# Kernel optimization log

Hardware: AMD Instinct MI355X
Metric: run time of the kernel (lower is better)

Reference implementation:

```python
import jax, jax.numpy as jnp
import numpy as np

D_IN = 1024
D_OUT = 1024
N_HEADS = 16
HEAD_DIM = D_IN // N_HEADS


def setup_inputs() -> dict:
    key = jax.random.key(0)
    k0, k1, k2, k3, k4, k5 = jax.random.split(key, 6)
    s = 1.0 / np.sqrt(D_IN)
    return {
        "input_embeddings": jax.random.normal(k0, (4, 2048, D_IN), dtype=jnp.float32),
        "Wq": jax.random.normal(k1, (D_IN, D_IN), dtype=jnp.float32) * s,
        "Wk": jax.random.normal(k2, (D_IN, D_IN), dtype=jnp.float32) * s,
        "Wv": jax.random.normal(k3, (D_IN, D_IN), dtype=jnp.float32) * s,
        "Wo": jax.random.normal(k4, (D_IN, D_OUT), dtype=jnp.float32) * s,
        "bo": jax.random.normal(k5, (D_OUT,), dtype=jnp.float32) * 0.01,
    }


def reference(input_embeddings, Wq, Wk, Wv, Wo, bo):
    B, T, D = input_embeddings.shape
    x = input_embeddings
    # QKV projections (no bias), split into heads: (B, H, T, hd)
    def split(y):
        return y.reshape(B, T, N_HEADS, HEAD_DIM).transpose(0, 2, 1, 3)
    Q = split(x @ Wq)
    K = split(x @ Wk)
    V = split(x @ Wv)
    scale = 1.0 / np.sqrt(HEAD_DIM)
    scores = jnp.einsum("bhqd,bhkd->bhqk", Q, K) * scale  # (B,H,T,T)
    causal = jnp.tril(jnp.ones((T, T), dtype=bool))
    scores = jnp.where(causal, scores, -jnp.inf)
    probs = jax.nn.softmax(scores, axis=-1)  # dropout p=0 -> identity
    out = jnp.einsum("bhqk,bhkd->bhqd", probs, V)
    out = out.transpose(0, 2, 1, 3).reshape(B, T, D)
    return out @ Wo + bo
```

## Files before the change

### kernel.cpp

```cpp
#include <hip/hip_runtime.h>
#include <hip/hip_bf16.h>
#include <math.h>

typedef __attribute__((ext_vector_type(8))) short short8;
typedef __attribute__((ext_vector_type(4))) float f32x4;

#define MFMA_BF16 __builtin_amdgcn_mfma_f32_16x16x32_bf16

static constexpr int Dm = 1024;
static constexpr int Tm = 2048;
static constexpr int Bb = 4;
static constexpr int NHm = 16;
static constexpr int HDm = 64;
static constexpr int Mtot = Bb * Tm;
static constexpr int NKT = Tm / 64;
static constexpr float kQScale = 0.125f * 1.4426950408889634f;

__device__ __forceinline__ unsigned short f2bf(float f) {
  unsigned int u = __float_as_uint(f);
  u += 0x7FFFu + ((u >> 16) & 1u);
  return (unsigned short)(u >> 16);
}

__device__ __forceinline__ float fexp2(float x) {
  float r;
  asm("v_exp_f32 %0, %1" : "=v"(r) : "v"(x));
  return r;
}

__device__ __forceinline__ void gload16(const void* g, void* l) {
  __builtin_amdgcn_global_load_lds((const __attribute__((address_space(1))) void*)g,
                                   (__attribute__((address_space(3))) void*)l, 16, 0, 0);
}

__global__ __launch_bounds__(256) void cvt_kernel(const float* __restrict__ src,
                                                  short* __restrict__ dst, int n) {
  int stride = gridDim.x * blockDim.x;
  for (int i = blockIdx.x * blockDim.x + threadIdx.x; i * 4 < n; i += stride) {
    float4 v = reinterpret_cast<const float4*>(src)[i];
    short4 o;
    o.x = (short)f2bf(v.x);
    o.y = (short)f2bf(v.y);
    o.z = (short)f2bf(v.z);
    o.w = (short)f2bf(v.w);
    reinterpret_cast<short4*>(dst)[i] = o;
  }
}

__global__ __launch_bounds__(256) void cvt_t_kernel(
    const float* __restrict__ W0, const float* __restrict__ W1,
    const float* __restrict__ W2, const float* __restrict__ W3,
    short* __restrict__ T0, short* __restrict__ T1,
    short* __restrict__ T2, short* __restrict__ T3) {
  const float* W = blockIdx.z == 0 ? W0 : blockIdx.z == 1 ? W1 : blockIdx.z == 2 ? W2 : W3;
  short* Wt = blockIdx.z == 0 ? T0 : blockIdx.z == 1 ? T1 : blockIdx.z == 2 ? T2 : T3;
  __shared__ __align__(16) short T[64 * 72];
  const int tid = threadIdx.x;
  const int k0 = blockIdx.y * 64, n0 = blockIdx.x * 64;
#pragma unroll
  for (int p = 0; p < 4; ++p) {
    int idx = tid + p * 256;
    int kr = idx >> 4, c4 = (idx & 15) * 4;
    float4 v = *reinterpret_cast<const float4*>(W + (size_t)(k0 + kr) * Dm + n0 + c4);
    T[(c4 + 0) * 72 + kr] = (short)f2bf(v.x);
    T[(c4 + 1) * 72 + kr] = (short)f2bf(v.y);
    T[(c4 + 2) * 72 + kr] = (short)f2bf(v.z);
    T[(c4 + 3) * 72 + kr] = (short)f2bf(v.w);
  }
  __syncthreads();
#pragma unroll
  for (int p = 0; p < 2; ++p) {
    int idx = tid + p * 256;
    int nr = idx >> 3, c8 = (idx & 7) * 8;
    *reinterpret_cast<short8*>(Wt + (size_t)(n0 + nr) * Dm + k0 + c8) =
        *reinterpret_cast<const short8*>(&T[nr * 72 + c8]);
  }
}

__device__ __forceinline__ void gemm_mainloop2(
    const short* __restrict__ A, const short* __restrict__ B,
    int m0, int n0, short* As, short* Bs, f32x4 acc[4][4], int tid) {
  const int lane = tid & 63;
  const int w = tid >> 6;
  const int wr = (w >> 1) * 64, wc = (w & 1) * 64;
  const int lr = lane & 15;
  const int g = lane >> 4;
  const int rowt = tid >> 2;
  const int csw = ((tid & 3) ^ ((tid >> 3) & 3)) * 8;

  auto stage = [&](int kt, int buf) {
#pragma unroll
    for (int p = 0; p < 2; ++p) {
      gload16(A + (size_t)(m0 + p * 64 + rowt) * Dm + kt * 32 + csw,
              &As[buf * 4096 + (p * 64 + w * 16) * 32]);
      gload16(B + (size_t)(n0 + p * 64 + rowt) * Dm + kt * 32 + csw,
              &Bs[buf * 4096 + (p * 64 + w * 16) * 32]);
    }
  };

  const int rsw = (lr >> 1) & 3;
  const int csel = (g ^ rsw) * 8;

  stage(0, 0);
  __syncthreads();
  for (int kt = 0; kt < Dm / 32; ++kt) {
    if (kt + 1 < Dm / 32) stage(kt + 1, (kt + 1) & 1);
    __builtin_amdgcn_sched_barrier(0);
    const int cur = kt & 1;
    short8 a[4], b[4];
#pragma unroll
    for (int mi = 0; mi < 4; ++mi)
      a[mi] = *reinterpret_cast<const short8*>(
          &As[cur * 4096 + (wr + mi * 16 + lr) * 32 + csel]);
#pragma unroll
    for (int ni = 0; ni < 4; ++ni)
      b[ni] = *reinterpret_cast<const short8*>(
          &Bs[cur * 4096 + (wc + ni * 16 + lr) * 32 + csel]);
#pragma unroll
    for (int mi = 0; mi < 4; ++mi)
#pragma unroll
      for (int ni = 0; ni < 4; ++ni)
        acc[mi][ni] = MFMA_BF16(a[mi], b[ni], acc[mi][ni], 0, 0, 0);
    __syncthreads();
  }
}

__global__ __launch_bounds__(256) void gemm_qkv_kernel(
    const short* __restrict__ Ags, const short* __restrict__ WT3,
    short* __restrict__ Qo, short* __restrict__ Ko, short* __restrict__ Vo) {
  __shared__ __align__(16) short As[2 * 128 * 32];
  __shared__ __align__(16) short Bs[2 * 128 * 32];
  const int tid = threadIdx.x;
  const int m0 = blockIdx.x * 128;
  const int n0g = blockIdx.y * 128;
  const int z = n0g >> 10;
  const int n0 = n0g & 1023;
  short* Co = z == 0 ? Qo : z == 1 ? Ko : Vo;

  f32x4 acc[4][4];
#pragma unroll
  for (int mi = 0; mi < 4; ++mi)
#pragma unroll
    for (int ni = 0; ni < 4; ++ni)
#pragma unroll
      for (int r = 0; r < 4; ++r) acc[mi][ni][r] = 0.f;

  gemm_mainloop2(Ags, WT3, m0, n0g, As, Bs, acc, tid);

  const int lane = tid & 63;
  const int w = tid >> 6;
  const int wr = (w >> 1) * 64, wc = (w & 1) * 64;
  const int g = lane >> 4, lr = lane & 15;
#pragma unroll
  for (int mi = 0; mi < 4; ++mi)
#pragma unroll
    for (int ni = 0; ni < 4; ++ni)
#pragma unroll
      for (int r = 0; r < 4; ++r) {
        int mg = m0 + wr + mi * 16 + g * 4 + r;
        int ng = n0 + wc + ni * 16 + lr;
        float v = acc[mi][ni][r];
        int b_ = mg >> 11, t_ = mg & 2047, h_ = ng >> 6, d_ = ng & 63;
        size_t bh = (size_t)(b_ * NHm + h_);
        if (z == 0) {
          Co[(bh * Tm + t_) * HDm + d_] = (short)f2bf(v * kQScale);
        } else if (z == 1) {
          Co[((bh * NKT + (t_ >> 6)) << 12) + (t_ & 63) * 64 + (d_ ^ ((t_ & 7) << 3))] =
              (short)f2bf(v);
        } else {
          Co[((bh * NKT + (t_ >> 6)) << 12) + d_ * 64 + ((t_ & 63) ^ ((d_ & 7) << 3))] =
              (short)f2bf(v);
        }
      }
}

__global__ __launch_bounds__(256) void gemm_out_kernel(
    const short* __restrict__ Ags, const short* __restrict__ Bts,
    float* __restrict__ Cf, const float* __restrict__ bias) {
  __shared__ __align__(16) short As[2 * 128 * 32];
  __shared__ __align__(16) short Bs[2 * 128 * 32];
  const int tid = threadIdx.x;
  const int m0 = blockIdx.x * 128;
  const int n0 = blockIdx.y * 128;

  f32x4 acc[4][4];
#pragma unroll
  for (int mi = 0; mi < 4; ++mi)
#pragma unroll
    for (int ni = 0; ni < 4; ++ni)
#pragma unroll
      for (int r = 0; r < 4; ++r) acc[mi][ni][r] = 0.f;

  gemm_mainloop2(Ags, Bts, m0, n0, As, Bs, acc, tid);

  const int lane = tid & 63;
  const int w = tid >> 6;
  const int wr = (w >> 1) * 64, wc = (w & 1) * 64;
  const int g = lane >> 4, lr = lane & 15;
#pragma unroll
  for (int mi = 0; mi < 4; ++mi)
#pragma unroll
    for (int ni = 0; ni < 4; ++ni)
#pragma unroll
      for (int r = 0; r < 4; ++r) {
        int mg = m0 + wr + mi * 16 + g * 4 + r;
        int ng = n0 + wc + ni * 16 + lr;
        Cf[(size_t)mg * Dm + ng] = acc[mi][ni][r] + bias[ng];
      }
}

__global__ __launch_bounds__(256) void attn_kernel(
    const short* __restrict__ Qg, const short* __restrict__ Kg,
    const short* __restrict__ Vg, short* __restrict__ Og) {
  __shared__ __align__(16) short Kl[3][64 * 64];
  __shared__ __align__(16) short Vl[3][64 * 64];
  __shared__ __align__(16) short Pl[4][32 * 72];
  const int tid = threadIdx.x;
  const int lane = tid & 63;
  const int w = tid >> 6;
  const int g = lane >> 4;
  const int lr = lane & 15;
  const int bh = blockIdx.x;
  const int pi = blockIdx.y;
  const short* Ks = Kg + ((size_t)bh * NKT << 12);
  const short* Vs = Vg + ((size_t)bh * NKT << 12);
  short* Pw = &Pl[w][0];
  const int b_ = bh >> 4, h_ = bh & 15;

  short8 ones;
#pragma unroll
  for (int j = 0; j < 8; ++j) ones[j] = (short)0x3F80;

  auto stage = [&](int t, int buf) {
#pragma unroll
    for (int i = 0; i < 2; ++i) {
      int ch = w * 2 + i;
      gload16(Ks + ((size_t)t << 12) + ch * 512 + lane * 8, &Kl[buf][ch * 512]);
      gload16(Vs + ((size_t)t << 12) + ch * 512 + lane * 8, &Vl[buf][ch * 512]);
    }
  };

  for (int pass = 0; pass < 2; ++pass) {
    const int qb = pass == 0 ? (15 - pi) : pi;
    const int q0 = qb * 128;
    const int qw = q0 + w * 32;
    const short* Qs = Qg + ((size_t)bh * Tm + q0) * HDm;

    short8 qf[2][2];
#pragma unroll
    for (int mi = 0; mi < 2; ++mi)
#pragma unroll
      for (int kk = 0; kk < 2; ++kk)
        qf[mi][kk] = *reinterpret_cast<const short8*>(
            Qs + (w * 32 + mi * 16 + lr) * HDm + kk * 32 + g * 8);

    f32x4 o[2][4], lacc[2];
#pragma unroll
    for (int mi = 0; mi < 2; ++mi)
#pragma unroll
      for (int r = 0; r < 4; ++r) {
        lacc[mi][r] = 0.f;
#pragma unroll
        for (int di = 0; di < 4; ++di) o[mi][di][r] = 0.f;
      }

    const int nt = q0 / 64 + 2;
    stage(0, 0);
    stage(1, 1);
    for (int t = 0; t < nt; ++t) {
      if (t < nt - 1) asm volatile("s_waitcnt vmcnt(4)" ::: "memory");
      else            asm volatile("s_waitcnt vmcnt(0)" ::: "memory");
      __builtin_amdgcn_s_barrier();
      __builtin_amdgcn_sched_barrier(0);
      if (t + 2 < nt) stage(t + 2, (t + 2) % 3);
      const int cur = t % 3;
      const int k0 = t * 64;
      const bool active = (k0 <= qw + 31);
      if (active) {
        short8 kf[2][4];
#pragma unroll
        for (int ni = 0; ni < 4; ++ni) {
          int row = ni * 16 + lr;
#pragma unroll
          for (int kk = 0; kk < 2; ++kk)
            kf[kk][ni] = *reinterpret_cast<const short8*>(
                &Kl[cur][row * 64 + ((kk * 32 + g * 8) ^ ((row & 7) << 3))]);
        }
        f32x4 s[2][4];
#pragma unroll
        for (int mi = 0; mi < 2; ++mi)
#pragma unroll
          for (int ni = 0; ni < 4; ++ni) {
            f32x4 acc;
#pragma unroll
            for (int r = 0; r < 4; ++r) acc[r] = 0.f;
            acc = MFMA_BF16(qf[mi][0], kf[0][ni], acc, 0, 0, 0);
            acc = MFMA_BF16(qf[mi][1], kf[1][ni], acc, 0, 0, 0);
            s[mi][ni] = acc;
          }
        if (k0 + 63 > qw) {
#pragma unroll
          for (int mi = 0; mi < 2; ++mi)
#pragma unroll
            for (int ni = 0; ni < 4; ++ni)
#pragma unroll
              for (int r = 0; r < 4; ++r)
                if (k0 + ni * 16 + lr > qw + mi * 16 + g * 4 + r) s[mi][ni][r] = -1e30f;
        }
#pragma unroll
        for (int mi = 0; mi < 2; ++mi)
#pragma unroll
          for (int ni = 0; ni < 4; ++ni)
#pragma unroll
            for (int r = 0; r < 4; ++r)
              Pw[(mi * 16 + g * 4 + r) * 72 + ((ni * 16 + lr) ^ (g << 4))] =
                  (short)f2bf(fexp2(s[mi][ni][r]));

#pragma unroll
        for (int kk = 0; kk < 2; ++kk) {
          short8 pf[2];
#pragma unroll
          for (int mi = 0; mi < 2; ++mi)
            pf[mi] = *reinterpret_cast<const short8*>(
                &Pw[(mi * 16 + lr) * 72 + ((kk * 32 + g * 8) ^ ((lr >> 2) << 4))]);
#pragma unroll
          for (int mi = 0; mi < 2; ++mi)
            lacc[mi] = MFMA_BF16(pf[mi], ones, lacc[mi], 0, 0, 0);
#pragma unroll
          for (int di = 0; di < 4; ++di) {
            int d = di * 16 + lr;
            short8 vf = *reinterpret_cast<const short8*>(
                &Vl[cur][d * 64 + ((kk * 32 + g * 8) ^ ((d & 7) << 3))]);
#pragma unroll
            for (int mi = 0; mi < 2; ++mi)
              o[mi][di] = MFMA_BF16(pf[mi], vf, o[mi][di], 0, 0, 0);
          }
        }
      }
    }
    __syncthreads();

#pragma unroll
    for (int mi = 0; mi < 2; ++mi)
#pragma unroll
      for (int di = 0; di < 4; ++di)
#pragma unroll
        for (int r = 0; r < 4; ++r) {
          float ov = o[mi][di][r] / lacc[mi][r];
          int qg = q0 + w * 32 + mi * 16 + g * 4 + r;
          int d_ = di * 16 + lr;
          Og[((size_t)b_ * Tm + qg) * Dm + h_ * HDm + d_] = (short)f2bf(ov);
        }
  }
}

extern "C" void kernel_launch(void* const* d_in, const int* in_sizes, int n_in,
                              void* d_out, int out_size, void* d_ws, size_t ws_size,
                              hipStream_t stream) {
  const float* X = (const float*)d_in[0];
  const float* Wq = (const float*)d_in[1];
  const float* Wk = (const float*)d_in[2];
  const float* Wv = (const float*)d_in[3];
  const float* Wo = (const float*)d_in[4];
  const float* bo = (const float*)d_in[5];
  float* out = (float*)d_out;

  char* ws = (char*)d_ws;
  short* Xb = (short*)ws;  ws += (size_t)Mtot * Dm * 2;
  short* Wqt = (short*)ws; ws += (size_t)Dm * Dm * 2;
  short* Wkt = (short*)ws; ws += (size_t)Dm * Dm * 2;
  short* Wvt = (short*)ws; ws += (size_t)Dm * Dm * 2;
  short* Wot = (short*)ws; ws += (size_t)Dm * Dm * 2;
  short* Qb = (short*)ws;  ws += (size_t)Mtot * Dm * 2;
  short* Kb = (short*)ws;  ws += (size_t)Mtot * Dm * 2;
  short* Vb = (short*)ws;  ws += (size_t)Mtot * Dm * 2;
  short* Ab = (short*)ws;  ws += (size_t)Mtot * Dm * 2;

  cvt_kernel<<<dim3(1024), dim3(256), 0, stream>>>(X, Xb, Mtot * Dm);
  cvt_t_kernel<<<dim3(16, 16, 4), dim3(256), 0, stream>>>(Wq, Wk, Wv, Wo, Wqt, Wkt, Wvt, Wot);

  gemm_qkv_kernel<<<dim3(Mtot / 128, 3 * Dm / 128), 256, 0, stream>>>(
      Xb, Wqt, Qb, Kb, Vb);

  attn_kernel<<<dim3(Bb * NHm, 8), 256, 0, stream>>>(Qb, Kb, Vb, Ab);

  gemm_out_kernel<<<dim3(Mtot / 128, Dm / 128), 256, 0, stream>>>(Ab, Wot, out, bo);
}
```

Before: 192.8 us.

## Load GEMM A operands directly into registers, stage only B through LDS

The QKV and output GEMM mainloops no longer stage A tiles in shared memory. Each wave loads its A fragments straight from global memory into double-buffered registers one k-step ahead, and only B goes through LDS via async loads. Synchronisation uses explicit barriers and vmcnt waits, and launch bounds request 4 blocks per CU. This halves LDS footprint and traffic to allow higher occupancy, but A global loads are no longer shared across the two waves that use the same rows, which doubles A reads from L2.

```diff
diff --git a/kernel.cpp b/kernel.cpp
--- a/kernel.cpp
+++ b/kernel.cpp
@@ -77,9 +77,35 @@
   }
 }
 
-__device__ __forceinline__ void gemm_mainloop2(
+#define GSTEP(KT, CUR, PF)                                                    \
+  {                                                                           \
+    __builtin_amdgcn_s_barrier();  \
+    if (PF) {                                                                 \
+      _Pragma("unroll") for (int mi = 0; mi < 4; ++mi)                        \
+          a[(CUR) ^ 1][mi] = *reinterpret_cast<const short8*>(                \
+              Ar[mi] + ((KT) + 1) * 32);                                      \
+      stageB((KT) + 1, (CUR) ^ 1);                                            \
+      __builtin_amdgcn_sched_barrier(0);                                      \
+      asm volatile("s_waitcnt vmcnt(6)" ::: "memory");                        \
+    } else {                                                                  \
+      asm volatile("s_waitcnt vmcnt(0)" ::: "memory");                        \
+    }                                                                         \
+    __builtin_amdgcn_s_barrier();                        \
+    __builtin_amdgcn_sched_barrier(0);                                        \
+    short8 b[4];                                                              \
+    _Pragma("unroll") for (int ni = 0; ni < 4; ++ni)                          \
+        b[ni] = *reinterpret_cast<const short8*>(                             \
+            &Bs[(CUR) * 4096 + (wc + ni * 16 + lr) * 32 + csel]);             \
+    _Pragma("unroll") for (int mi = 0; mi < 4; ++mi)                          \
+        _Pragma("unroll") for (int ni = 0; ni < 4; ++ni)                      \
+            acc[mi][ni] =                                                     \
+                MFMA_BF16(a[CUR][mi], b[ni], acc[mi][ni], 0, 0, 0);           \
+  }
+
+__device__ __forceinline__ void gemm_mainloopA(
     const short* __restrict__ A, const short* __restrict__ B,
-    int m0, int n0, short* As, short* Bs, f32x4 acc[4][4], int tid) {
+    int m0, int n0, short* Bs, f32x4 acc[4][4], int tid) {
+  constexpr int NT = Dm / 32;
   const int lane = tid & 63;
   const int w = tid >> 6;
   const int wr = (w >> 1) * 64, wc = (w & 1) * 64;
@@ -87,48 +113,38 @@
   const int g = lane >> 4;
   const int rowt = tid >> 2;
   const int csw = ((tid & 3) ^ ((tid >> 3) & 3)) * 8;
-
-  auto stage = [&](int kt, int buf) {
-#pragma unroll
-    for (int p = 0; p < 2; ++p) {
-      gload16(A + (size_t)(m0 + p * 64 + rowt) * Dm + kt * 32 + csw,
-              &As[buf * 4096 + (p * 64 + w * 16) * 32]);
-      gload16(B + (size_t)(n0 + p * 64 + rowt) * Dm + kt * 32 + csw,
-              &Bs[buf * 4096 + (p * 64 + w * 16) * 32]);
-    }
+  const short* Bsrc0 = B + (size_t)(n0 + rowt) * Dm + csw;
+  const short* Bsrc1 = B + (size_t)(n0 + 64 + rowt) * Dm + csw;
+  short* Bd0 = Bs + (w * 16) * 32;
+  short* Bd1 = Bs + (64 + w * 16) * 32;
+  auto stageB = [&](int kt, int buf) {
+    gload16(Bsrc0 + kt * 32, Bd0 + buf * 4096);
+    gload16(Bsrc1 + kt * 32, Bd1 + buf * 4096);
   };
-
-  const int rsw = (lr >> 1) & 3;
-  const int csel = (g ^ rsw) * 8;
-
-  stage(0, 0);
-  __syncthreads();
-  for (int kt = 0; kt < Dm / 32; ++kt) {
-    if (kt + 1 < Dm / 32) stage(kt + 1, (kt + 1) & 1);
-    __builtin_amdgcn_sched_barrier(0);
-    const int cur = kt & 1;
-    short8 a[4], b[4];
-#pragma unroll
-    for (int mi = 0; mi < 4; ++mi)
-      a[mi] = *reinterpret_cast<const short8*>(
-          &As[cur * 4096 + (wr + mi * 16 + lr) * 32 + csel]);
-#pragma unroll
-    for (int ni = 0; ni < 4; ++ni)
-      b[ni] = *reinterpret_cast<const short8*>(
-          &Bs[cur * 4096 + (wc + ni * 16 + lr) * 32 + csel]);
-#pragma unroll
-    for (int mi = 0; mi < 4; ++mi)
-#pragma unroll
-      for (int ni = 0; ni < 4; ++ni)
-        acc[mi][ni] = MFMA_BF16(a[mi], b[ni], acc[mi][ni], 0, 0, 0);
-    __syncthreads();
-  }
-}
-
-__global__ __launch_bounds__(256) void gemm_qkv_kernel(
+  const short* Ar[4];
+#pragma unroll
+  for (int mi = 0; mi < 4; ++mi)
+    Ar[mi] = A + (size_t)(m0 + wr + mi * 16 + lr) * Dm + g * 8;
+
+  const int csel = (g ^ ((lr >> 1) & 3)) * 8;
+
+  short8 a[2][4];
+#pragma unroll
+  for (int mi = 0; mi < 4; ++mi)
+    a[0][mi] = *reinterpret_cast<const short8*>(Ar[mi]);
+  stageB(0, 0);
+
+  for (int kt2 = 0; kt2 < NT - 2; kt2 += 2) {
+    GSTEP(kt2, 0, 1);
+    GSTEP(kt2 + 1, 1, 1);
+  }
+  GSTEP(NT - 2, 0, 1);
+  GSTEP(NT - 1, 1, 0);
+}
+
+__global__ __launch_bounds__(256, 4) void gemm_qkv_kernel(
     const short* __restrict__ Ags, const short* __restrict__ WT3,
     short* __restrict__ Qo, short* __restrict__ Ko, short* __restrict__ Vo) {
-  __shared__ __align__(16) short As[2 * 128 * 32];
   __shared__ __align__(16) short Bs[2 * 128 * 32];
   const int tid = threadIdx.x;
   const int m0 = blockIdx.x * 128;
@@ -145,7 +161,7 @@
 #pragma unroll
       for (int r = 0; r < 4; ++r) acc[mi][ni][r] = 0.f;
 
-  gemm_mainloop2(Ags, WT3, m0, n0g, As, Bs, acc, tid);
+  gemm_mainloopA(Ags, WT3, m0, n0g, Bs, acc, tid);
 
   const int lane = tid & 63;
   const int w = tid >> 6;
@@ -174,10 +190,9 @@
       }
 }
 
-__global__ __launch_bounds__(256) void gemm_out_kernel(
+__global__ __launch_bounds__(256, 4) void gemm_out_kernel(
     const short* __restrict__ Ags, const short* __restrict__ Bts,
     float* __restrict__ Cf, const float* __restrict__ bias) {
-  __shared__ __align__(16) short As[2 * 128 * 32];
   __shared__ __align__(16) short Bs[2 * 128 * 32];
   const int tid = threadIdx.x;
   const int m0 = blockIdx.x * 128;
@@ -191,7 +206,7 @@
 #pragma unroll
       for (int r = 0; r < 4; ++r) acc[mi][ni][r] = 0.f;
 
-  gemm_mainloop2(Ags, Bts, m0, n0, As, Bs, acc, tid);
+  gemm_mainloopA(Ags, Bts, m0, n0, Bs, acc, tid);
 
   const int lane = tid & 63;
   const int w = tid >> 6;
```

Result: slower. 290.3 us (+50.5%).

## Make GEMM waves independent with private LDS tiles and vmcnt waits

Applied to the files above, without the earlier changes.

Replaces the 256-thread block GEMMs, which shared LDS tiles across four waves, with a 128-thread kernel in which each wave stages and consumes its own 64x64 A/B tiles in private LDS buffers. Block-wide __syncthreads are replaced by per-wave s_waitcnt vmcnt counters, so waves no longer stall on one another. The QKV and output GEMMs are merged into one templated kernel. In exchange, each wave reloads B tiles the other wave also loads, which raises global/L2 traffic and cuts data reuse. The correctness of the hand-written vmcnt counts depends on how the compiler schedules the loads.

```diff
diff --git a/kernel.cpp b/kernel.cpp
--- a/kernel.cpp
+++ b/kernel.cpp
@@ -77,135 +77,103 @@
   }
 }
 
-__device__ __forceinline__ void gemm_mainloop2(
-    const short* __restrict__ A, const short* __restrict__ B,
-    int m0, int n0, short* As, short* Bs, f32x4 acc[4][4], int tid) {
+template <int MODE>
+__global__ __launch_bounds__(128, 4) void gemm_wave_kernel(
+    const short* __restrict__ Ags, const short* __restrict__ Bts,
+    short* __restrict__ Qo, short* __restrict__ Ko, short* __restrict__ Vo,
+    float* __restrict__ Cf, const float* __restrict__ bias) {
+  __shared__ __align__(16) short L[2][2][2][64 * 32];
+  constexpr int NT = Dm / 32;
+  const int tid = threadIdx.x;
   const int lane = tid & 63;
   const int w = tid >> 6;
-  const int wr = (w >> 1) * 64, wc = (w & 1) * 64;
+  const int g = lane >> 4;
   const int lr = lane & 15;
-  const int g = lane >> 4;
-  const int rowt = tid >> 2;
-  const int csw = ((tid & 3) ^ ((tid >> 3) & 3)) * 8;
+  const int m0 = blockIdx.x * 128 + w * 64;
+  const int n0g = blockIdx.y * 64;
+  const int srow = lane >> 2;
+  const int sch = ((lane & 3) ^ ((lane >> 3) & 3)) * 8;
+  const short* Asrc[4];
+  const short* Bsrc[4];
+#pragma unroll
+  for (int j = 0; j < 4; ++j) {
+    Asrc[j] = Ags + (size_t)(m0 + j * 16 + srow) * Dm + sch;
+    Bsrc[j] = Bts + (size_t)(n0g + j * 16 + srow) * Dm + sch;
+  }
 
   auto stage = [&](int kt, int buf) {
 #pragma unroll
-    for (int p = 0; p < 2; ++p) {
-      gload16(A + (size_t)(m0 + p * 64 + rowt) * Dm + kt * 32 + csw,
-              &As[buf * 4096 + (p * 64 + w * 16) * 32]);
-      gload16(B + (size_t)(n0 + p * 64 + rowt) * Dm + kt * 32 + csw,
-              &Bs[buf * 4096 + (p * 64 + w * 16) * 32]);
+    for (int j = 0; j < 4; ++j) {
+      gload16(Asrc[j] + kt * 32, &L[w][buf][0][j * 512]);
+      gload16(Bsrc[j] + kt * 32, &L[w][buf][1][j * 512]);
     }
   };
 
-  const int rsw = (lr >> 1) & 3;
-  const int csel = (g ^ rsw) * 8;
+  f32x4 acc[4][4];
+#pragma unroll
+  for (int mi = 0; mi < 4; ++mi)
+#pragma unroll
+    for (int ni = 0; ni < 4; ++ni)
+#pragma unroll
+      for (int r = 0; r < 4; ++r) acc[mi][ni][r] = 0.f;
+
+  const int csel = (g ^ ((lr >> 1) & 3)) * 8;
 
   stage(0, 0);
-  __syncthreads();
-  for (int kt = 0; kt < Dm / 32; ++kt) {
-    if (kt + 1 < Dm / 32) stage(kt + 1, (kt + 1) & 1);
+  for (int kt = 0; kt < NT; ++kt) {
+    if (kt + 1 < NT) {
+      stage(kt + 1, (kt + 1) & 1);
+      __builtin_amdgcn_sched_barrier(0);
+      asm volatile("s_waitcnt vmcnt(8)" ::: "memory");
+    } else {
+      asm volatile("s_waitcnt vmcnt(0)" ::: "memory");
+    }
     __builtin_amdgcn_sched_barrier(0);
     const int cur = kt & 1;
     short8 a[4], b[4];
 #pragma unroll
     for (int mi = 0; mi < 4; ++mi)
       a[mi] = *reinterpret_cast<const short8*>(
-          &As[cur * 4096 + (wr + mi * 16 + lr) * 32 + csel]);
+          &L[w][cur][0][(mi * 16 + lr) * 32 + csel]);
 #pragma unroll
     for (int ni = 0; ni < 4; ++ni)
       b[ni] = *reinterpret_cast<const short8*>(
-          &Bs[cur * 4096 + (wc + ni * 16 + lr) * 32 + csel]);
+          &L[w][cur][1][(ni * 16 + lr) * 32 + csel]);
 #pragma unroll
     for (int mi = 0; mi < 4; ++mi)
 #pragma unroll
       for (int ni = 0; ni < 4; ++ni)
         acc[mi][ni] = MFMA_BF16(a[mi], b[ni], acc[mi][ni], 0, 0, 0);
-    __syncthreads();
-  }
-}
-
-__global__ __launch_bounds__(256) void gemm_qkv_kernel(
-    const short* __restrict__ Ags, const short* __restrict__ WT3,
-    short* __restrict__ Qo, short* __restrict__ Ko, short* __restrict__ Vo) {
-  __shared__ __align__(16) short As[2 * 128 * 32];
-  __shared__ __align__(16) short Bs[2 * 128 * 32];
-  const int tid = threadIdx.x;
-  const int m0 = blockIdx.x * 128;
-  const int n0g = blockIdx.y * 128;
+  }
+
   const int z = n0g >> 10;
   const int n0 = n0g & 1023;
-  short* Co = z == 0 ? Qo : z == 1 ? Ko : Vo;
-
-  f32x4 acc[4][4];
+  short* Co = (MODE == 0) ? (z == 0 ? Qo : z == 1 ? Ko : Vo) : nullptr;
 #pragma unroll
   for (int mi = 0; mi < 4; ++mi)
 #pragma unroll
     for (int ni = 0; ni < 4; ++ni)
 #pragma unroll
-      for (int r = 0; r < 4; ++r) acc[mi][ni][r] = 0.f;
-
-  gemm_mainloop2(Ags, WT3, m0, n0g, As, Bs, acc, tid);
-
-  const int lane = tid & 63;
-  const int w = tid >> 6;
-  const int wr = (w >> 1) * 64, wc = (w & 1) * 64;
-  const int g = lane >> 4, lr = lane & 15;
-#pragma unroll
-  for (int mi = 0; mi < 4; ++mi)
-#pragma unroll
-    for (int ni = 0; ni < 4; ++ni)
-#pragma unroll
       for (int r = 0; r < 4; ++r) {
-        int mg = m0 + wr + mi * 16 + g * 4 + r;
-        int ng = n0 + wc + ni * 16 + lr;
+        int mg = m0 + mi * 16 + g * 4 + r;
         float v = acc[mi][ni][r];
-        int b_ = mg >> 11, t_ = mg & 2047, h_ = ng >> 6, d_ = ng & 63;
-        size_t bh = (size_t)(b_ * NHm + h_);
-        if (z == 0) {
-          Co[(bh * Tm + t_) * HDm + d_] = (short)f2bf(v * kQScale);
-        } else if (z == 1) {
-          Co[((bh * NKT + (t_ >> 6)) << 12) + (t_ & 63) * 64 + (d_ ^ ((t_ & 7) << 3))] =
-              (short)f2bf(v);
+        if (MODE == 1) {
+          int ng = n0g + ni * 16 + lr;
+          Cf[(size_t)mg * Dm + ng] = v + bias[ng];
         } else {
-          Co[((bh * NKT + (t_ >> 6)) << 12) + d_ * 64 + ((t_ & 63) ^ ((d_ & 7) << 3))] =
-              (short)f2bf(v);
-        }
-      }
-}
-
-__global__ __launch_bounds__(256) void gemm_out_kernel(
-    const short* __restrict__ Ags, const short* __restrict__ Bts,
-    float* __restrict__ Cf, const float* __restrict__ bias) {
-  __shared__ __align__(16) short As[2 * 128 * 32];
-  __shared__ __align__(16) short Bs[2 * 128 * 32];
-  const int tid = threadIdx.x;
-  const int m0 = blockIdx.x * 128;
-  const int n0 = blockIdx.y * 128;
-
-  f32x4 acc[4][4];
-#pragma unroll
-  for (int mi = 0; mi < 4; ++mi)
-#pragma unroll
-    for (int ni = 0; ni < 4; ++ni)
-#pragma unroll
-      for (int r = 0; r < 4; ++r) acc[mi][ni][r] = 0.f;
-
-  gemm_mainloop2(Ags, Bts, m0, n0, As, Bs, acc, tid);
-
-  const int lane = tid & 63;
-  const int w = tid >> 6;
-  const int wr = (w >> 1) * 64, wc = (w & 1) * 64;
-  const int g = lane >> 4, lr = lane & 15;
-#pragma unroll
-  for (int mi = 0; mi < 4; ++mi)
-#pragma unroll
-    for (int ni = 0; ni < 4; ++ni)
-#pragma unroll
-      for (int r = 0; r < 4; ++r) {
-        int mg = m0 + wr + mi * 16 + g * 4 + r;
-        int ng = n0 + wc + ni * 16 + lr;
-        Cf[(size_t)mg * Dm + ng] = acc[mi][ni][r] + bias[ng];
+          int ng = n0 + ni * 16 + lr;
+          int b_ = mg >> 11, t_ = mg & 2047, h_ = ng >> 6, d_ = ng & 63;
+          size_t bh = (size_t)(b_ * NHm + h_);
+          if (z == 0) {
+            Co[(bh * Tm + t_) * HDm + d_] = (short)f2bf(v * kQScale);
+          } else if (z == 1) {
+            Co[((bh * NKT + (t_ >> 6)) << 12) + (t_ & 63) * 64 + (d_ ^ ((t_ & 7) << 3))] =
+                (short)f2bf(v);
+          } else {
+            Co[((bh * NKT + (t_ >> 6)) << 12) + d_ * 64 + ((t_ & 63) ^ ((d_ & 7) << 3))] =
+                (short)f2bf(v);
+          }
+        }
       }
 }
 
@@ -379,10 +347,11 @@
   cvt_kernel<<<dim3(1024), dim3(256), 0, stream>>>(X, Xb, Mtot * Dm);
   cvt_t_kernel<<<dim3(16, 16, 4), dim3(256), 0, stream>>>(Wq, Wk, Wv, Wo, Wqt, Wkt, Wvt, Wot);
 
-  gemm_qkv_kernel<<<dim3(Mtot / 128, 3 * Dm / 128), 256, 0, stream>>>(
-      Xb, Wqt, Qb, Kb, Vb);
+  gemm_wave_kernel<0><<<dim3(Mtot / 128, 3 * Dm / 64), 128, 0, stream>>>(
+      Xb, Wqt, Qb, Kb, Vb, nullptr, nullptr);
 
   attn_kernel<<<dim3(Bb * NHm, 8), 256, 0, stream>>>(Qb, Kb, Vb, Ab);
 
-  gemm_out_kernel<<<dim3(Mtot / 128, Dm / 128), 256, 0, stream>>>(Ab, Wot, out, bo);
-}
+  gemm_wave_kernel<1><<<dim3(Mtot / 128, Dm / 64), 128, 0, stream>>>(
+      Ab, Wot, nullptr, nullptr, nullptr, out, bo);
+}
```

Result: slower. 228.6 us (+18.6%).
